# Kernel tuning notes

Hardware: AMD Instinct MI355X
Metric: run time of the kernel (lower is better)

The kernel has to match this reference:

```python
import jax, jax.numpy as jnp
import numpy as np

NUM_LONGTERM_MEM = 16  # config.num_longterm_mem


def setup_inputs() -> dict:
    key = jax.random.key(0)
    ks = jax.random.split(key, 9)
    B, T, C, H = 32, 2048, 768, 1536
    s = 0.02
    return {
        "x": jax.random.normal(ks[0], (B, T, C), jnp.float32),
        "Wq": jax.random.normal(ks[1], (C, C), jnp.float32) * s,
        "bq": jax.random.normal(ks[2], (C,), jnp.float32) * s,
        "W0": jax.random.normal(ks[3], (B, H, C), jnp.float32) * s,
        "b0": jax.random.normal(ks[4], (B, H), jnp.float32) * s,
        "W1": jax.random.normal(ks[5], (B, C, H), jnp.float32) * s,
        "b1": jax.random.normal(ks[6], (B, C), jnp.float32) * s,
        "Wo": jax.random.normal(ks[7], (C, C), jnp.float32) * s,
        "bo": jax.random.normal(ks[8], (C,), jnp.float32) * s,
    }


def reference(x, Wq, bq, W0, b0, W1, b1, Wo, bo):
    # x: [B, T, C]. Per-sample memory MLP weights W0 [B,H,C], W1 [B,C,H].
    B, T, C = x.shape
    L = NUM_LONGTERM_MEM
    # query projection (nn.Linear: x @ W^T + b)
    q = jnp.einsum("btc,dc->btd", x, Wq) + bq                       # [B,T,C]
    # per-sample 2-layer memory MLP with SiLU
    h = jax.nn.silu(jnp.einsum("btc,bhc->bth", q, W0) + b0[:, None, :])  # [B,T,H]
    mem = jnp.einsum("bth,bch->btc", h, W1) + b1[:, None, :]        # [B,T,C]
    # adaptive_avg_pool1d over T -> L (T divisible by L => uniform window mean)
    pooled = mem.reshape(B, L, T // L, C).mean(axis=2)              # [B,L,C]
    # output projection
    return jnp.einsum("blc,dc->bld", pooled, Wo) + bo               # [B,L,C]
```

## Files before the change

### kernel.cpp

```cpp
#include <hip/hip_runtime.h>
#include <stdint.h>

#define B_ 32
#define T_ 2048
#define C_ 768
#define H_ 1536
#define L_ 16

typedef unsigned short u16;
typedef __bf16 bf16x8 __attribute__((ext_vector_type(8)));
typedef float f32x4 __attribute__((ext_vector_type(4)));

__device__ __forceinline__ u16 f2bf(float f) {
    union { float f; uint32_t u; } v; v.f = f;
    uint32_t r = (v.u + 0x7fffu + ((v.u >> 16) & 1u)) >> 16;
    return (u16)r;
}

__device__ __forceinline__ float wave_sum(float v) {
    v += __shfl_xor(v, 1);  v += __shfl_xor(v, 2);  v += __shfl_xor(v, 4);
    v += __shfl_xor(v, 8);  v += __shfl_xor(v, 16); v += __shfl_xor(v, 32);
    return v;
}

__global__ void k_cvt(const float* __restrict__ in, u16* __restrict__ out, int n4) {
    int stride = gridDim.x * blockDim.x;
    for (int i = blockIdx.x * blockDim.x + threadIdx.x; i < n4; i += stride) {
        float4 v = reinterpret_cast<const float4*>(in)[i];
        ushort4 o;
        o.x = f2bf(v.x); o.y = f2bf(v.y); o.z = f2bf(v.z); o.w = f2bf(v.w);
        reinterpret_cast<ushort4*>(out)[i] = o;
    }
}

__device__ __forceinline__ void gload16(const u16* g, u16* l) {
    __builtin_amdgcn_global_load_lds((const __attribute__((address_space(1))) void*)g,
                                     (__attribute__((address_space(3))) void*)l, 16, 0, 0);
}

#define PH_SYNC() do { __builtin_amdgcn_s_barrier(); \
    asm volatile("s_waitcnt lgkmcnt(0)" ::: "memory"); \
    __builtin_amdgcn_sched_barrier(0); } while (0)
#define PH_END() do { __builtin_amdgcn_sched_barrier(0); __builtin_amdgcn_s_barrier(); } while (0)

template <int EPI>
__global__ __launch_bounds__(512, 2) void k_gemm8(const u16* __restrict__ Aall,
                                                  const u16* __restrict__ Ball,
                                                  const float* __restrict__ biasall,
                                                  u16* __restrict__ qout,
                                                  float* __restrict__ ph) {
    __shared__ u16 sm[65536];
    const int t = threadIdx.x;
    const int w = t >> 6, lane = t & 63;
    const int wr = w >> 2, wc = w & 3;
    const int l15 = lane & 15, kq = lane >> 4, cx = lane & 7;

    const int gx = gridDim.x, gy = gridDim.y;
    const int nwg = gx * gy * gridDim.z;
    int flat = blockIdx.x + gx * (blockIdx.y + gy * blockIdx.z);
    if ((nwg & 7) == 0) flat = (flat & 7) * (nwg >> 3) + (flat >> 3);
    const int bx = flat % gx;
    const int tmp = flat / gx;
    const int by = tmp % gy;
    const int bz = tmp / gy;

    const int n0 = bx * 256;
    const int m0 = by * 256;
    const u16* A; const u16* Bm; const float* bias;
    if constexpr (EPI == 0) {
        A = Aall + (size_t)m0 * C_;
        Bm = Ball + (size_t)n0 * C_;
        bias = biasall + n0;
    } else {
        A = Aall + ((size_t)bz * T_ + m0) * C_;
        Bm = Ball + ((size_t)bz * H_ + n0) * C_;
        bias = biasall + (size_t)bz * H_ + n0;
    }

    const int rl = (w << 4) + (lane >> 3);
    const int cs = (((lane & 7) ^ ((lane >> 3) & 7)) << 3);
    const int ldst = (w << 10);

    auto stA = [&](int kt, int h) {
        const u16* g = A + (size_t)(h * 128 + rl) * C_ + kt * 64 + cs;
        u16* l = sm + (kt & 1) * 32768 + h * 8192 + ldst;
        gload16(g, l);
        gload16(g + 8 * C_, l + 512);
    };
    auto stB = [&](int kt, int h) {
        const u16* g = Bm + (size_t)(h * 128 + rl) * C_ + kt * 64 + cs;
        u16* l = sm + (kt & 1) * 32768 + 16384 + h * 8192 + ldst;
        gload16(g, l);
        gload16(g + 8 * C_, l + 512);
    };

    f32x4 acc[8][4];
#pragma unroll
    for (int m = 0; m < 8; ++m)
#pragma unroll
        for (int n = 0; n < 4; ++n) acc[m][n] = (f32x4){0.f, 0.f, 0.f, 0.f};

    bf16x8 a0[4][2], a1[4][2], bfr[2][2];

    auto rdA = [&](bf16x8 (&a)[4][2], int bt, int mq) {
        const u16* Ah = sm + bt * 32768 + wr * 8192;
#pragma unroll
        for (int mm = 0; mm < 4; ++mm) {
            const u16* rp = Ah + ((mq * 4 + mm) * 16 + l15) * 64;
#pragma unroll
            for (int ks = 0; ks < 2; ++ks)
                a[mm][ks] = *reinterpret_cast<const bf16x8*>(rp + ((((ks << 2) + kq) ^ cx) << 3));
        }
    };
    auto rdB = [&](int bt, int qn) {
        const u16* Bh = sm + bt * 32768 + 16384 + (wc >> 1) * 8192;
        const int cb = (wc & 1) * 64 + qn * 32;
#pragma unroll
        for (int nn = 0; nn < 2; ++nn) {
            const u16* cp = Bh + (cb + nn * 16 + l15) * 64;
#pragma unroll
            for (int ks = 0; ks < 2; ++ks)
                bfr[nn][ks] = *reinterpret_cast<const bf16x8*>(cp + ((((ks << 2) + kq) ^ cx) << 3));
        }
    };
    auto mma16 = [&](bf16x8 (&a)[4][2], int mq, int qn) {
        __builtin_amdgcn_s_setprio(1);
#pragma unroll
        for (int ks = 0; ks < 2; ++ks)
#pragma unroll
            for (int mm = 0; mm < 4; ++mm)
#pragma unroll
                for (int nn = 0; nn < 2; ++nn)
                    acc[mq * 4 + mm][qn * 2 + nn] = __builtin_amdgcn_mfma_f32_16x16x32_bf16(
                        a[mm][ks], bfr[nn][ks], acc[mq * 4 + mm][qn * 2 + nn], 0, 0, 0);
        __builtin_amdgcn_s_setprio(0);
    };

    stA(0, 0); stA(0, 1); stB(0, 0); stB(0, 1);
    stA(1, 0); stA(1, 1); stB(1, 0);
    asm volatile("s_waitcnt vmcnt(6)" ::: "memory");
    __builtin_amdgcn_s_barrier();

#pragma unroll 1
    for (int kt = 0; kt < 12; ++kt) {
        const int bt = kt & 1;
        rdA(a0, bt, 0);
        rdB(bt, 0);
        if (kt + 1 < 12) stB(kt + 1, 1);
        PH_SYNC();
        mma16(a0, 0, 0);
        PH_END();
        rdA(a1, bt, 1);
        PH_SYNC();
        mma16(a1, 1, 0);
        PH_END();
        rdB(bt, 1);
        if (kt + 2 < 12) stA(kt + 2, 0);
        PH_SYNC();
        mma16(a0, 0, 1);
        PH_END();
        if (kt + 2 < 12) {
            stA(kt + 2, 1);
            stB(kt + 2, 0);
            asm volatile("s_waitcnt vmcnt(6)" ::: "memory");
        } else {
            asm volatile("s_waitcnt vmcnt(0)" ::: "memory");
        }
        __builtin_amdgcn_s_barrier();
        __builtin_amdgcn_sched_barrier(0);
        mma16(a1, 1, 1);
        PH_END();
    }

    if constexpr (EPI == 0) {
        const int colb = n0 + wc * 64 + l15;
        const int rowb = m0 + wr * 128 + (kq << 2);
        float bv[4];
#pragma unroll
        for (int n = 0; n < 4; ++n) bv[n] = bias[wc * 64 + n * 16 + l15];
#pragma unroll
        for (int m = 0; m < 8; ++m)
#pragma unroll
            for (int r = 0; r < 4; ++r) {
                size_t ro = (size_t)(rowb + m * 16 + r) * C_;
#pragma unroll
                for (int n = 0; n < 4; ++n)
                    qout[ro + colb + n * 16] = f2bf(acc[m][n][r] + bv[n]);
            }
    } else {
        const int lwin = by * 2 + wr;
#pragma unroll
        for (int n = 0; n < 4; ++n) {
            int cloc = wc * 64 + n * 16 + l15;
            float bv = bias[cloc];
            float s = 0.f;
#pragma unroll
            for (int m = 0; m < 8; ++m)
#pragma unroll
                for (int r = 0; r < 4; ++r) {
                    float v = acc[m][n][r] + bv;
                    s += v / (1.f + __expf(-v));
                }
            s += __shfl_xor(s, 16);
            s += __shfl_xor(s, 32);
            if (kq == 0)
                ph[((size_t)bz * L_ + lwin) * H_ + n0 + cloc] = s * (1.f / 128.f);
        }
    }
}

__device__ __forceinline__ void stage_bf16_gload(const u16* gtile, int ld, u16* Ts,
                                                 int w, int lane) {
    const int r_in = lane >> 3;
    const int c0   = (lane & 7) << 3;
#pragma unroll
    for (int j = 0; j < 4; ++j) {
        int row = ((w << 2) + j) * 8 + r_in;
        const u16* g = gtile + (size_t)row * ld + c0;
        u16* l = Ts + (((w << 2) + j) << 9);
        gload16(g, l);
    }
}

__device__ __forceinline__ void stage_f32_cvt(const float* gtile, int ld, u16* Ts, int t) {
#pragma unroll
    for (int i = 0; i < 8; ++i) {
        int slot = t + (i << 8);
        int row  = slot >> 4;
        int c4   = (slot & 15) << 2;
        float4 v = *reinterpret_cast<const float4*>(gtile + (size_t)row * ld + c4);
        ushort4 o;
        o.x = f2bf(v.x); o.y = f2bf(v.y); o.z = f2bf(v.z); o.w = f2bf(v.w);
        *reinterpret_cast<ushort4*>(&Ts[row * 64 + c4]) = o;
    }
}

__device__ __forceinline__ void mfma_tile(const u16* As, const u16* Bs,
                                          f32x4 (&acc)[4][4], int wr, int wc, int lane) {
#pragma unroll
    for (int ks = 0; ks < 2; ++ks) {
        const int ko = (ks << 5) + ((lane >> 4) << 3);
        bf16x8 a[4], b[4];
#pragma unroll
        for (int m = 0; m < 4; ++m)
            a[m] = *reinterpret_cast<const bf16x8*>(&As[(wr * 64 + m * 16 + (lane & 15)) * 64 + ko]);
#pragma unroll
        for (int n = 0; n < 4; ++n)
            b[n] = *reinterpret_cast<const bf16x8*>(&Bs[(wc * 64 + n * 16 + (lane & 15)) * 64 + ko]);
#pragma unroll
        for (int m = 0; m < 4; ++m)
#pragma unroll
            for (int n = 0; n < 4; ++n)
                acc[m][n] = __builtin_amdgcn_mfma_f32_16x16x32_bf16(a[m], b[n], acc[m][n], 0, 0, 0);
    }
}

__global__ __launch_bounds__(256, 2) void k_gemm1(const float* __restrict__ x,
                                                  const u16* __restrict__ Wqb,
                                                  const float* __restrict__ bq,
                                                  u16* __restrict__ qb) {
    __shared__ u16 As[128 * 64];
    __shared__ u16 Bs[128 * 64];
    const int t = threadIdx.x, w = t >> 6, lane = t & 63;
    const int wr = w >> 1, wc = w & 1;
    const int m0 = blockIdx.y * 128;
    const int n0 = blockIdx.x * 128;

    f32x4 acc[4][4];
#pragma unroll
    for (int m = 0; m < 4; ++m)
#pragma unroll
        for (int n = 0; n < 4; ++n) acc[m][n] = (f32x4){0.f, 0.f, 0.f, 0.f};

    for (int kt = 0; kt < C_ / 64; ++kt) {
        stage_f32_cvt(x + (size_t)m0 * C_ + kt * 64, C_, As, t);
        stage_bf16_gload(Wqb + (size_t)n0 * C_ + kt * 64, C_, Bs, w, lane);
        __syncthreads();
        mfma_tile(As, Bs, acc, wr, wc, lane);
        __syncthreads();
    }

    const int r0 = m0 + wr * 64 + ((lane >> 4) << 2);
    const int cb = n0 + wc * 64 + (lane & 15);
#pragma unroll
    for (int n = 0; n < 4; ++n) {
        int c = cb + n * 16;
        float bb = bq[c];
#pragma unroll
        for (int m = 0; m < 4; ++m)
#pragma unroll
            for (int r = 0; r < 4; ++r)
                qb[(size_t)(r0 + m * 16 + r) * C_ + c] = f2bf(acc[m][n][r] + bb);
    }
}

template <bool BPRE>
__global__ __launch_bounds__(256, 2) void k_gemm2(const u16* __restrict__ qb,
                                                  const u16* __restrict__ W0b,
                                                  const float* __restrict__ W0f,
                                                  const float* __restrict__ b0,
                                                  float* __restrict__ ph) {
    __shared__ u16 As[128 * 64];
    __shared__ u16 Bs[128 * 64];
    __shared__ float Ps[2][128];
    const int t = threadIdx.x, w = t >> 6, lane = t & 63;
    const int wr = w >> 1, wc = w & 1;
    const int b  = blockIdx.z;
    const int mt = blockIdx.y;
    const int n0 = blockIdx.x * 128;
    const u16* Abase = qb + ((size_t)b * T_ + mt * 128) * C_;

    f32x4 acc[4][4];
#pragma unroll
    for (int m = 0; m < 4; ++m)
#pragma unroll
        for (int n = 0; n < 4; ++n) acc[m][n] = (f32x4){0.f, 0.f, 0.f, 0.f};

    for (int kt = 0; kt < C_ / 64; ++kt) {
        stage_bf16_gload(Abase + kt * 64, C_, As, w, lane);
        if (BPRE)
            stage_bf16_gload(W0b + ((size_t)b * H_ + n0) * C_ + kt * 64, C_, Bs, w, lane);
        else
            stage_f32_cvt(W0f + ((size_t)b * H_ + n0) * C_ + kt * 64, C_, Bs, t);
        __syncthreads();
        mfma_tile(As, Bs, acc, wr, wc, lane);
        __syncthreads();
    }

    float s[4];
#pragma unroll
    for (int n = 0; n < 4; ++n) {
        int c = n0 + wc * 64 + n * 16 + (lane & 15);
        float bb = b0[b * H_ + c];
        float sum = 0.f;
#pragma unroll
        for (int m = 0; m < 4; ++m)
#pragma unroll
            for (int r = 0; r < 4; ++r) {
                float v = acc[m][n][r] + bb;
                sum += v / (1.f + __expf(-v));
            }
        sum += __shfl_xor(sum, 16);
        sum += __shfl_xor(sum, 32);
        s[n] = sum;
    }
    if (lane < 16) {
#pragma unroll
        for (int n = 0; n < 4; ++n) Ps[wr][wc * 64 + n * 16 + lane] = s[n];
    }
    __syncthreads();
    if (t < 128)
        ph[((size_t)b * L_ + mt) * H_ + n0 + t] = (Ps[0][t] + Ps[1][t]) * (1.f / 128.f);
}

__global__ __launch_bounds__(256) void k_3a(const float* __restrict__ ph,
                                            const float* __restrict__ W1,
                                            const float* __restrict__ b1,
                                            float* __restrict__ pooled) {
    const int t = threadIdx.x, w = t >> 6, lane = t & 63;
    const int b  = blockIdx.y;
    const int cb = blockIdx.x * 16 + w * 4;

    float acc[4][16];
#pragma unroll
    for (int g = 0; g < 4; ++g)
#pragma unroll
        for (int l = 0; l < 16; ++l) acc[g][l] = 0.f;

    for (int i = 0; i < H_ / 256; ++i) {
        int h0 = i * 256 + lane * 4;
        float4 wv[4];
#pragma unroll
        for (int g = 0; g < 4; ++g)
            wv[g] = *reinterpret_cast<const float4*>(W1 + ((size_t)b * C_ + cb + g) * H_ + h0);
#pragma unroll
        for (int l = 0; l < 16; ++l) {
            float4 pv = *reinterpret_cast<const float4*>(ph + ((size_t)b * L_ + l) * H_ + h0);
#pragma unroll
            for (int g = 0; g < 4; ++g)
                acc[g][l] += wv[g].x * pv.x + wv[g].y * pv.y + wv[g].z * pv.z + wv[g].w * pv.w;
        }
    }
#pragma unroll
    for (int g = 0; g < 4; ++g)
#pragma unroll
        for (int l = 0; l < 16; ++l) acc[g][l] = wave_sum(acc[g][l]);

    if (lane < 16) {
#pragma unroll
        for (int g = 0; g < 4; ++g)
            pooled[((size_t)b * L_ + lane) * C_ + cb + g] = acc[g][lane] + b1[b * C_ + cb + g];
    }
}

__global__ __launch_bounds__(256) void k_3b(const float* __restrict__ pooled,
                                            const float* __restrict__ Wo,
                                            const float* __restrict__ bo,
                                            float* __restrict__ out) {
    __shared__ __align__(16) float ps[4 * 768];
    const int t = threadIdx.x, w = t >> 6, lane = t & 63;
    const int rr0 = blockIdx.x * 4;

    for (int idx = t; idx < 4 * 768; idx += 256)
        ps[idx] = pooled[(size_t)rr0 * 768 + idx];
    __syncthreads();

    for (int d = w; d < 768; d += 4) {
        float a0 = 0.f, a1 = 0.f, a2 = 0.f, a3 = 0.f;
#pragma unroll
        for (int i = 0; i < 3; ++i) {
            int c = i * 256 + lane * 4;
            float4 wv = *reinterpret_cast<const float4*>(Wo + (size_t)d * 768 + c);
            float4 p0 = *reinterpret_cast<const float4*>(&ps[0 * 768 + c]);
            float4 p1 = *reinterpret_cast<const float4*>(&ps[1 * 768 + c]);
            float4 p2 = *reinterpret_cast<const float4*>(&ps[2 * 768 + c]);
            float4 p3 = *reinterpret_cast<const float4*>(&ps[3 * 768 + c]);
            a0 += wv.x * p0.x + wv.y * p0.y + wv.z * p0.z + wv.w * p0.w;
            a1 += wv.x * p1.x + wv.y * p1.y + wv.z * p1.z + wv.w * p1.w;
            a2 += wv.x * p2.x + wv.y * p2.y + wv.z * p2.z + wv.w * p2.w;
            a3 += wv.x * p3.x + wv.y * p3.y + wv.z * p3.z + wv.w * p3.w;
        }
        a0 = wave_sum(a0); a1 = wave_sum(a1); a2 = wave_sum(a2); a3 = wave_sum(a3);
        if (lane == 0) {
            float bb = bo[d];
            out[(size_t)(rr0 + 0) * 768 + d] = a0 + bb;
            out[(size_t)(rr0 + 1) * 768 + d] = a1 + bb;
            out[(size_t)(rr0 + 2) * 768 + d] = a2 + bb;
            out[(size_t)(rr0 + 3) * 768 + d] = a3 + bb;
        }
    }
}

extern "C" void kernel_launch(void* const* d_in, const int* in_sizes, int n_in,
                              void* d_out, int out_size, void* d_ws, size_t ws_size,
                              hipStream_t stream) {
    const float* x  = (const float*)d_in[0];
    const float* Wq = (const float*)d_in[1];
    const float* bq = (const float*)d_in[2];
    const float* W0 = (const float*)d_in[3];
    const float* b0 = (const float*)d_in[4];
    const float* W1 = (const float*)d_in[5];
    const float* b1 = (const float*)d_in[6];
    const float* Wo = (const float*)d_in[7];
    const float* bo = (const float*)d_in[8];
    float* out = (float*)d_out;

    char* p = (char*)d_ws;
    size_t off = 0;
    auto carve = [&](size_t bytes) -> char* {
        char* r = p + off;
        off += (bytes + 255) & ~(size_t)255;
        return r;
    };
    u16*   qb     = (u16*)carve((size_t)B_ * T_ * C_ * 2);
    u16*   Wqb    = (u16*)carve((size_t)C_ * C_ * 2);
    float* ph     = (float*)carve((size_t)B_ * L_ * H_ * 4);
    float* pooled = (float*)carve((size_t)B_ * L_ * C_ * 4);

    const size_t xb_bytes  = (size_t)B_ * T_ * C_ * 2;
    const size_t w0b_bytes = (size_t)B_ * H_ * C_ * 2;

    if (off + xb_bytes <= ws_size) {
        u16* xb  = (u16*)carve(xb_bytes);
        u16* W0b = xb;

        k_cvt<<<dim3(2048), 256, 0, stream>>>(x, xb, B_ * T_ * C_ / 4);
        k_cvt<<<dim3(64), 256, 0, stream>>>(Wq, Wqb, C_ * C_ / 4);
        k_gemm8<0><<<dim3(C_ / 256, (B_ * T_) / 256), 512, 0, stream>>>(xb, Wqb, bq, qb, nullptr);
        k_cvt<<<dim3(2048), 256, 0, stream>>>(W0, W0b, B_ * H_ * C_ / 4);
        k_gemm8<1><<<dim3(H_ / 256, T_ / 256, B_), 512, 0, stream>>>(qb, W0b, b0, nullptr, ph);
    } else {
        u16* W0b = nullptr;
        if (off + w0b_bytes <= ws_size) W0b = (u16*)carve(w0b_bytes);

        k_cvt<<<dim3(64), 256, 0, stream>>>(Wq, Wqb, C_ * C_ / 4);
        if (W0b)
            k_cvt<<<dim3(2048), 256, 0, stream>>>(W0, W0b, B_ * H_ * C_ / 4);
        k_gemm1<<<dim3(C_ / 128, (B_ * T_) / 128), 256, 0, stream>>>(x, Wqb, bq, qb);
        if (W0b)
            k_gemm2<true><<<dim3(H_ / 128, L_, B_), 256, 0, stream>>>(qb, W0b, nullptr, b0, ph);
        else
            k_gemm2<false><<<dim3(H_ / 128, L_, B_), 256, 0, stream>>>(qb, nullptr, W0, b0, ph);
    }

    k_3a<<<dim3(C_ / 16, B_), 256, 0, stream>>>(ph, W1, b1, pooled);
    k_3b<<<dim3(B_ * L_ / 4), 256, 0, stream>>>(pooled, Wo, bo, out);
}
```

Measured before the change: 647.6 us.

## Restructure GEMM main loop with fewer barriers and precomputed LDS read pointers

Replaces the four-phase ping-pong schedule (barrier plus lgkmcnt wait around each MFMA cluster) with two barriers per k-tile. A, B and A1 fragments are loaded upfront with precomputed swizzled base pointers, and global-to-LDS loads are regrouped (whole B tile for kt+1, whole A tile for kt+2). The loop is unrolled by two so the buffer index is a constant. This cuts synchronization and address arithmetic, at the cost of relying on the compiler's scheduling rather than explicit phase interleaving, and it changes when LDS buffers get overwritten, which could introduce races.

```diff
diff --git a/kernel.cpp b/kernel.cpp
--- a/kernel.cpp
+++ b/kernel.cpp
@@ -37,11 +37,6 @@
     __builtin_amdgcn_global_load_lds((const __attribute__((address_space(1))) void*)g,
                                      (__attribute__((address_space(3))) void*)l, 16, 0, 0);
 }
-
-#define PH_SYNC() do { __builtin_amdgcn_s_barrier(); \
-    asm volatile("s_waitcnt lgkmcnt(0)" ::: "memory"); \
-    __builtin_amdgcn_sched_barrier(0); } while (0)
-#define PH_END() do { __builtin_amdgcn_sched_barrier(0); __builtin_amdgcn_s_barrier(); } while (0)
 
 template <int EPI>
 __global__ __launch_bounds__(512, 2) void k_gemm8(const u16* __restrict__ Aall,
@@ -102,26 +97,50 @@
 
     bf16x8 a0[4][2], a1[4][2], bfr[2][2];
 
-    auto rdA = [&](bf16x8 (&a)[4][2], int bt, int mq) {
-        const u16* Ah = sm + bt * 32768 + wr * 8192;
-#pragma unroll
-        for (int mm = 0; mm < 4; ++mm) {
-            const u16* rp = Ah + ((mq * 4 + mm) * 16 + l15) * 64;
-#pragma unroll
-            for (int ks = 0; ks < 2; ++ks)
-                a[mm][ks] = *reinterpret_cast<const bf16x8*>(rp + ((((ks << 2) + kq) ^ cx) << 3));
-        }
-    };
-    auto rdB = [&](int bt, int qn) {
-        const u16* Bh = sm + bt * 32768 + 16384 + (wc >> 1) * 8192;
-        const int cb = (wc & 1) * 64 + qn * 32;
-#pragma unroll
-        for (int nn = 0; nn < 2; ++nn) {
-            const u16* cp = Bh + (cb + nn * 16 + l15) * 64;
-#pragma unroll
-            for (int ks = 0; ks < 2; ++ks)
-                bfr[nn][ks] = *reinterpret_cast<const bf16x8*>(cp + ((((ks << 2) + kq) ^ cx) << 3));
-        }
+    const int koff0 = ((kq ^ cx) << 3);
+    const int koff1 = (((4 + kq) ^ cx) << 3);
+    const u16* vA0 = sm + wr * 8192 + l15 * 64 + koff0;
+    const u16* vA1 = sm + wr * 8192 + l15 * 64 + koff1;
+    const u16* vB0 = sm + 16384 + (wc >> 1) * 8192 + (wc & 1) * 4096 + l15 * 64 + koff0;
+    const u16* vB1 = sm + 16384 + (wc >> 1) * 8192 + (wc & 1) * 4096 + l15 * 64 + koff1;
+
+    auto rdAB0 = [&](int bt) {
+        const u16* A0 = vA0 + bt * 32768;
+        const u16* A1 = vA1 + bt * 32768;
+        const u16* B0 = vB0 + bt * 32768;
+        const u16* B1 = vB1 + bt * 32768;
+        bfr[0][0] = *reinterpret_cast<const bf16x8*>(B0);
+        bfr[1][0] = *reinterpret_cast<const bf16x8*>(B0 + 1024);
+        a0[0][0] = *reinterpret_cast<const bf16x8*>(A0);
+        a0[1][0] = *reinterpret_cast<const bf16x8*>(A0 + 1024);
+        a0[2][0] = *reinterpret_cast<const bf16x8*>(A0 + 2048);
+        a0[3][0] = *reinterpret_cast<const bf16x8*>(A0 + 3072);
+        bfr[0][1] = *reinterpret_cast<const bf16x8*>(B1);
+        bfr[1][1] = *reinterpret_cast<const bf16x8*>(B1 + 1024);
+        a0[0][1] = *reinterpret_cast<const bf16x8*>(A1);
+        a0[1][1] = *reinterpret_cast<const bf16x8*>(A1 + 1024);
+        a0[2][1] = *reinterpret_cast<const bf16x8*>(A1 + 2048);
+        a0[3][1] = *reinterpret_cast<const bf16x8*>(A1 + 3072);
+    };
+    auto rdA1 = [&](int bt) {
+        const u16* A0 = vA0 + bt * 32768 + 4096;
+        const u16* A1 = vA1 + bt * 32768 + 4096;
+        a1[0][0] = *reinterpret_cast<const bf16x8*>(A0);
+        a1[1][0] = *reinterpret_cast<const bf16x8*>(A0 + 1024);
+        a1[2][0] = *reinterpret_cast<const bf16x8*>(A0 + 2048);
+        a1[3][0] = *reinterpret_cast<const bf16x8*>(A0 + 3072);
+        a1[0][1] = *reinterpret_cast<const bf16x8*>(A1);
+        a1[1][1] = *reinterpret_cast<const bf16x8*>(A1 + 1024);
+        a1[2][1] = *reinterpret_cast<const bf16x8*>(A1 + 2048);
+        a1[3][1] = *reinterpret_cast<const bf16x8*>(A1 + 3072);
+    };
+    auto rdB1 = [&](int bt) {
+        const u16* B0 = vB0 + bt * 32768 + 2048;
+        const u16* B1 = vB1 + bt * 32768 + 2048;
+        bfr[0][0] = *reinterpret_cast<const bf16x8*>(B0);
+        bfr[1][0] = *reinterpret_cast<const bf16x8*>(B0 + 1024);
+        bfr[0][1] = *reinterpret_cast<const bf16x8*>(B1);
+        bfr[1][1] = *reinterpret_cast<const bf16x8*>(B1 + 1024);
     };
     auto mma16 = [&](bf16x8 (&a)[4][2], int mq, int qn) {
         __builtin_amdgcn_s_setprio(1);
@@ -136,40 +155,32 @@
         __builtin_amdgcn_s_setprio(0);
     };
 
+    auto ktile = [&](int kt, int bt) {
+        rdAB0(bt);
+        rdA1(bt);
+        if (kt + 1 < 12) { stB(kt + 1, 0); stB(kt + 1, 1); }
+        mma16(a0, 0, 0);
+        mma16(a1, 1, 0);
+        __builtin_amdgcn_s_barrier();
+        rdB1(bt);
+        const bool st = (kt + 2 < 12);
+        if (st) { stA(kt + 2, 0); stA(kt + 2, 1); }
+        mma16(a0, 0, 1);
+        mma16(a1, 1, 1);
+        if (st) asm volatile("s_waitcnt vmcnt(4)" ::: "memory");
+        else    asm volatile("s_waitcnt vmcnt(0)" ::: "memory");
+        __builtin_amdgcn_s_barrier();
+    };
+
     stA(0, 0); stA(0, 1); stB(0, 0); stB(0, 1);
-    stA(1, 0); stA(1, 1); stB(1, 0);
-    asm volatile("s_waitcnt vmcnt(6)" ::: "memory");
+    stA(1, 0); stA(1, 1);
+    asm volatile("s_waitcnt vmcnt(4)" ::: "memory");
     __builtin_amdgcn_s_barrier();
 
 #pragma unroll 1
-    for (int kt = 0; kt < 12; ++kt) {
-        const int bt = kt & 1;
-        rdA(a0, bt, 0);
-        rdB(bt, 0);
-        if (kt + 1 < 12) stB(kt + 1, 1);
-        PH_SYNC();
-        mma16(a0, 0, 0);
-        PH_END();
-        rdA(a1, bt, 1);
-        PH_SYNC();
-        mma16(a1, 1, 0);
-        PH_END();
-        rdB(bt, 1);
-        if (kt + 2 < 12) stA(kt + 2, 0);
-        PH_SYNC();
-        mma16(a0, 0, 1);
-        PH_END();
-        if (kt + 2 < 12) {
-            stA(kt + 2, 1);
-            stB(kt + 2, 0);
-            asm volatile("s_waitcnt vmcnt(6)" ::: "memory");
-        } else {
-            asm volatile("s_waitcnt vmcnt(0)" ::: "memory");
-        }
-        __builtin_amdgcn_s_barrier();
-        __builtin_amdgcn_sched_barrier(0);
-        mma16(a1, 1, 1);
-        PH_END();
+    for (int ktb = 0; ktb < 12; ktb += 2) {
+        ktile(ktb, 0);
+        ktile(ktb + 1, 1);
     }
 
     if constexpr (EPI == 0) {
```

Measured after the change: 624.9 us. -3.5%, faster.

## Triple-buffer A tiles in GEMM and fuse bf16 conversions into one launch

Applied to the files above, without the earlier changes.

The GEMM kernel moves to a triple-buffered A tile and double-buffered B tile in shared memory (160KB). The old multi-phase barrier choreography is replaced by one barrier per k-step, with precomputed swizzled LDS base pointers. The three fp32-to-bf16 conversion launches are merged into a single kernel that splits its blocks across the three tensors. When workspace allows, x and W0 get separate buffers so all conversions run up front. The goal is to cut launch overhead and synchronisation stalls. The cost is higher LDS use, which may reduce occupancy at two blocks per CU and change how loads overlap with MFMA work.

```diff
diff --git a/kernel.cpp b/kernel.cpp
--- a/kernel.cpp
+++ b/kernel.cpp
@@ -33,23 +33,35 @@
     }
 }
 
+__global__ void k_cvt3(const float* __restrict__ s0, u16* __restrict__ d0, int n0,
+                       const float* __restrict__ s1, u16* __restrict__ d1, int n1,
+                       const float* __restrict__ s2, u16* __restrict__ d2, int n2,
+                       int e0, int e1) {
+    const float* s; u16* d; int n, b0, nb;
+    if (blockIdx.x < (unsigned)e0)      { s = s0; d = d0; n = n0; b0 = 0;  nb = e0; }
+    else if (blockIdx.x < (unsigned)e1) { s = s1; d = d1; n = n1; b0 = e0; nb = e1 - e0; }
+    else                      { s = s2; d = d2; n = n2; b0 = e1; nb = gridDim.x - e1; }
+    int stride = nb * blockDim.x;
+    for (int i = (blockIdx.x - b0) * blockDim.x + threadIdx.x; i < n; i += stride) {
+        float4 v = reinterpret_cast<const float4*>(s)[i];
+        ushort4 o;
+        o.x = f2bf(v.x); o.y = f2bf(v.y); o.z = f2bf(v.z); o.w = f2bf(v.w);
+        reinterpret_cast<ushort4*>(d)[i] = o;
+    }
+}
+
 __device__ __forceinline__ void gload16(const u16* g, u16* l) {
     __builtin_amdgcn_global_load_lds((const __attribute__((address_space(1))) void*)g,
                                      (__attribute__((address_space(3))) void*)l, 16, 0, 0);
 }
 
-#define PH_SYNC() do { __builtin_amdgcn_s_barrier(); \
-    asm volatile("s_waitcnt lgkmcnt(0)" ::: "memory"); \
-    __builtin_amdgcn_sched_barrier(0); } while (0)
-#define PH_END() do { __builtin_amdgcn_sched_barrier(0); __builtin_amdgcn_s_barrier(); } while (0)
-
 template <int EPI>
-__global__ __launch_bounds__(512, 2) void k_gemm8(const u16* __restrict__ Aall,
+__global__ __launch_bounds__(512, 2) void k_gemm9(const u16* __restrict__ Aall,
                                                   const u16* __restrict__ Ball,
                                                   const float* __restrict__ biasall,
                                                   u16* __restrict__ qout,
                                                   float* __restrict__ ph) {
-    __shared__ u16 sm[65536];
+    __shared__ u16 sm[81920];
     const int t = threadIdx.x;
     const int w = t >> 6, lane = t & 63;
     const int wr = w >> 2, wc = w & 3;
@@ -81,17 +93,23 @@
     const int cs = (((lane & 7) ^ ((lane >> 3) & 7)) << 3);
     const int ldst = (w << 10);
 
-    auto stA = [&](int kt, int h) {
-        const u16* g = A + (size_t)(h * 128 + rl) * C_ + kt * 64 + cs;
-        u16* l = sm + (kt & 1) * 32768 + h * 8192 + ldst;
-        gload16(g, l);
-        gload16(g + 8 * C_, l + 512);
-    };
-    auto stB = [&](int kt, int h) {
-        const u16* g = Bm + (size_t)(h * 128 + rl) * C_ + kt * 64 + cs;
-        u16* l = sm + (kt & 1) * 32768 + 16384 + h * 8192 + ldst;
-        gload16(g, l);
-        gload16(g + 8 * C_, l + 512);
+    auto stA = [&](int kt, int buf) {
+#pragma unroll
+        for (int h = 0; h < 2; ++h) {
+            const u16* g = A + (size_t)(h * 128 + rl) * C_ + kt * 64 + cs;
+            u16* l = sm + buf * 16384 + h * 8192 + ldst;
+            gload16(g, l);
+            gload16(g + 8 * C_, l + 512);
+        }
+    };
+    auto stB = [&](int kt, int buf) {
+#pragma unroll
+        for (int h = 0; h < 2; ++h) {
+            const u16* g = Bm + (size_t)(h * 128 + rl) * C_ + kt * 64 + cs;
+            u16* l = sm + 49152 + buf * 16384 + h * 8192 + ldst;
+            gload16(g, l);
+            gload16(g + 8 * C_, l + 512);
+        }
     };
 
     f32x4 acc[8][4];
@@ -102,25 +120,37 @@
 
     bf16x8 a0[4][2], a1[4][2], bfr[2][2];
 
-    auto rdA = [&](bf16x8 (&a)[4][2], int bt, int mq) {
-        const u16* Ah = sm + bt * 32768 + wr * 8192;
+    const int koff0 = ((kq ^ cx) << 3);
+    const int koff1 = (((4 + kq) ^ cx) << 3);
+    const u16* aB0 = sm + wr * 8192 + l15 * 64 + koff0;
+    const u16* aB1 = sm + wr * 8192 + l15 * 64 + koff1;
+    const u16* bB0 = sm + 49152 + (wc >> 1) * 8192 + (wc & 1) * 4096 + l15 * 64 + koff0;
+    const u16* bB1 = sm + 49152 + (wc >> 1) * 8192 + (wc & 1) * 4096 + l15 * 64 + koff1;
+
+    auto rdB0 = [&](int off) {
+        bfr[0][0] = *reinterpret_cast<const bf16x8*>(bB0 + off);
+        bfr[1][0] = *reinterpret_cast<const bf16x8*>(bB0 + off + 1024);
+        bfr[0][1] = *reinterpret_cast<const bf16x8*>(bB1 + off);
+        bfr[1][1] = *reinterpret_cast<const bf16x8*>(bB1 + off + 1024);
+    };
+    auto rdB1 = [&](int off) {
+        bfr[0][0] = *reinterpret_cast<const bf16x8*>(bB0 + off + 2048);
+        bfr[1][0] = *reinterpret_cast<const bf16x8*>(bB0 + off + 3072);
+        bfr[0][1] = *reinterpret_cast<const bf16x8*>(bB1 + off + 2048);
+        bfr[1][1] = *reinterpret_cast<const bf16x8*>(bB1 + off + 3072);
+    };
+    auto rdA0 = [&](int off) {
 #pragma unroll
         for (int mm = 0; mm < 4; ++mm) {
-            const u16* rp = Ah + ((mq * 4 + mm) * 16 + l15) * 64;
-#pragma unroll
-            for (int ks = 0; ks < 2; ++ks)
-                a[mm][ks] = *reinterpret_cast<const bf16x8*>(rp + ((((ks << 2) + kq) ^ cx) << 3));
-        }
-    };
-    auto rdB = [&](int bt, int qn) {
-        const u16* Bh = sm + bt * 32768 + 16384 + (wc >> 1) * 8192;
-        const int cb = (wc & 1) * 64 + qn * 32;
-#pragma unroll
-        for (int nn = 0; nn < 2; ++nn) {
-            const u16* cp = Bh + (cb + nn * 16 + l15) * 64;
-#pragma unroll
-            for (int ks = 0; ks < 2; ++ks)
-                bfr[nn][ks] = *reinterpret_cast<const bf16x8*>(cp + ((((ks << 2) + kq) ^ cx) << 3));
+            a0[mm][0] = *reinterpret_cast<const bf16x8*>(aB0 + off + mm * 1024);
+            a0[mm][1] = *reinterpret_cast<const bf16x8*>(aB1 + off + mm * 1024);
+        }
+    };
+    auto rdA1 = [&](int off) {
+#pragma unroll
+        for (int mm = 0; mm < 4; ++mm) {
+            a1[mm][0] = *reinterpret_cast<const bf16x8*>(aB0 + off + 4096 + mm * 1024);
+            a1[mm][1] = *reinterpret_cast<const bf16x8*>(aB1 + off + 4096 + mm * 1024);
         }
     };
     auto mma16 = [&](bf16x8 (&a)[4][2], int mq, int qn) {
@@ -136,40 +166,33 @@
         __builtin_amdgcn_s_setprio(0);
     };
 
-    stA(0, 0); stA(0, 1); stB(0, 0); stB(0, 1);
-    stA(1, 0); stA(1, 1); stB(1, 0);
-    asm volatile("s_waitcnt vmcnt(6)" ::: "memory");
+    stA(0, 0); stB(0, 0); stA(1, 1);
+    asm volatile("s_waitcnt vmcnt(4)" ::: "memory");
     __builtin_amdgcn_s_barrier();
 
+    int ba = 0;
 #pragma unroll 1
     for (int kt = 0; kt < 12; ++kt) {
-        const int bt = kt & 1;
-        rdA(a0, bt, 0);
-        rdB(bt, 0);
-        if (kt + 1 < 12) stB(kt + 1, 1);
-        PH_SYNC();
+        const int bb = kt & 1;
+        int ban = ba + 2; if (ban >= 3) ban -= 3;
+        const bool s2 = (kt + 2 < 12);
+        if (kt + 1 < 12) stB(kt + 1, bb ^ 1);
+        if (s2) stA(kt + 2, ban);
+        const int aoff = ba * 16384;
+        const int boff = bb * 16384;
+        rdB0(boff);
+        rdA0(aoff);
+        rdA1(aoff);
         mma16(a0, 0, 0);
-        PH_END();
-        rdA(a1, bt, 1);
-        PH_SYNC();
         mma16(a1, 1, 0);
-        PH_END();
-        rdB(bt, 1);
-        if (kt + 2 < 12) stA(kt + 2, 0);
-        PH_SYNC();
+        __builtin_amdgcn_sched_barrier(0);
+        rdB1(boff);
         mma16(a0, 0, 1);
-        PH_END();
-        if (kt + 2 < 12) {
-            stA(kt + 2, 1);
-            stB(kt + 2, 0);
-            asm volatile("s_waitcnt vmcnt(6)" ::: "memory");
-        } else {
-            asm volatile("s_waitcnt vmcnt(0)" ::: "memory");
-        }
+        mma16(a1, 1, 1);
+        if (s2) asm volatile("s_waitcnt vmcnt(4)" ::: "memory");
+        else    asm volatile("s_waitcnt vmcnt(0)" ::: "memory");
         __builtin_amdgcn_s_barrier();
-        __builtin_amdgcn_sched_barrier(0);
-        mma16(a1, 1, 1);
-        PH_END();
+        ba = (ba + 1 == 3) ? 0 : ba + 1;
     }
 
     if constexpr (EPI == 0) {
@@ -460,22 +483,32 @@
     const size_t xb_bytes  = (size_t)B_ * T_ * C_ * 2;
     const size_t w0b_bytes = (size_t)B_ * H_ * C_ * 2;
 
-    if (off + xb_bytes <= ws_size) {
+    const int n4x  = B_ * T_ * C_ / 4;
+    const int n4wq = C_ * C_ / 4;
+    const int n4w0 = B_ * H_ * C_ / 4;
+
+    if (off + xb_bytes + w0b_bytes <= ws_size) {
+        u16* xb  = (u16*)carve(xb_bytes);
+        u16* W0b = (u16*)carve(w0b_bytes);
+        k_cvt3<<<dim3(3072), 256, 0, stream>>>(x, xb, n4x, Wq, Wqb, n4wq,
+                                               W0, W0b, n4w0, 1744, 1768);
+        k_gemm9<0><<<dim3(C_ / 256, (B_ * T_) / 256), 512, 0, stream>>>(xb, Wqb, bq, qb, nullptr);
+        k_gemm9<1><<<dim3(H_ / 256, T_ / 256, B_), 512, 0, stream>>>(qb, W0b, b0, nullptr, ph);
+    } else if (off + xb_bytes <= ws_size) {
         u16* xb  = (u16*)carve(xb_bytes);
         u16* W0b = xb;
-
-        k_cvt<<<dim3(2048), 256, 0, stream>>>(x, xb, B_ * T_ * C_ / 4);
-        k_cvt<<<dim3(64), 256, 0, stream>>>(Wq, Wqb, C_ * C_ / 4);
-        k_gemm8<0><<<dim3(C_ / 256, (B_ * T_) / 256), 512, 0, stream>>>(xb, Wqb, bq, qb, nullptr);
-        k_cvt<<<dim3(2048), 256, 0, stream>>>(W0, W0b, B_ * H_ * C_ / 4);
-        k_gemm8<1><<<dim3(H_ / 256, T_ / 256, B_), 512, 0, stream>>>(qb, W0b, b0, nullptr, ph);
+        k_cvt3<<<dim3(3072), 256, 0, stream>>>(x, xb, n4x, Wq, Wqb, n4wq,
+                                               nullptr, nullptr, 0, 3040, 3072);
+        k_gemm9<0><<<dim3(C_ / 256, (B_ * T_) / 256), 512, 0, stream>>>(xb, Wqb, bq, qb, nullptr);
+        k_cvt<<<dim3(2048), 256, 0, stream>>>(W0, W0b, n4w0);
+        k_gemm9<1><<<dim3(H_ / 256, T_ / 256, B_), 512, 0, stream>>>(qb, W0b, b0, nullptr, ph);
     } else {
         u16* W0b = nullptr;
         if (off + w0b_bytes <= ws_size) W0b = (u16*)carve(w0b_bytes);
 
-        k_cvt<<<dim3(64), 256, 0, stream>>>(Wq, Wqb, C_ * C_ / 4);
+        k_cvt<<<dim3(64), 256, 0, stream>>>(Wq, Wqb, n4wq);
         if (W0b)
-            k_cvt<<<dim3(2048), 256, 0, stream>>>(W0, W0b, B_ * H_ * C_ / 4);
+            k_cvt<<<dim3(2048), 256, 0, stream>>>(W0, W0b, n4w0);
         k_gemm1<<<dim3(C_ / 128, (B_ * T_) / 128), 256, 0, stream>>>(x, Wqb, bq, qb);
         if (W0b)
             k_gemm2<true><<<dim3(H_ / 128, L_, B_), 256, 0, stream>>>(qb, W0b, nullptr, b0, ph);
```

Measured after the change: 623.8 us. 3.7% less time.
